# Performance work log

Measured on AMD Instinct MI355X. Metric: run time of the kernel, lower is better.

## Reference

```python
import jax, jax.numpy as jnp
import numpy as np

N_P, N_A, D, H, E = 200000, 100000, 64, 32, 1000000


def setup_inputs() -> dict:
    key = jax.random.key(0)
    ks = jax.random.split(key, 32)
    inp = {}
    inp["x_paper"] = jax.random.normal(ks[0], (N_P, D), jnp.float32)
    inp["x_author"] = jax.random.normal(ks[1], (N_A, D), jnp.float32)
    inp["cites_src"] = jax.random.randint(ks[2], (E,), 0, N_P, jnp.int32)
    inp["cites_dst"] = jax.random.randint(ks[3], (E,), 0, N_P, jnp.int32)
    inp["writes_src"] = jax.random.randint(ks[4], (E,), 0, N_A, jnp.int32)
    inp["writes_dst"] = jax.random.randint(ks[5], (E,), 0, N_P, jnp.int32)
    inp["rev_src"] = jax.random.randint(ks[6], (E,), 0, N_P, jnp.int32)
    inp["rev_dst"] = jax.random.randint(ks[7], (E,), 0, N_A, jnp.int32)
    # per-relation SAGEConv params; layer 1: D->H, layer 2: H->H
    i = 8
    for layer, din in ((1, D), (2, H)):
        for rel in ("cites", "writes", "rev"):
            inp[f"W{layer}l_{rel}"] = 0.1 * jax.random.normal(ks[i], (din, H), jnp.float32); i += 1
            inp[f"W{layer}r_{rel}"] = 0.1 * jax.random.normal(ks[i], (din, H), jnp.float32); i += 1
            inp[f"b{layer}_{rel}"] = 0.01 * jax.random.normal(ks[i], (H,), jnp.float32); i += 1
    return inp


def _sage(x_src, x_dst, src, dst, Wl, Wr, b, n_dst):
    # PyG SAGEConv (aggr='mean'): lin_l(mean of source msgs) + lin_r(x_dst) + bias
    msg = x_src[src]                                              # [E, d] gather
    s = jax.ops.segment_sum(msg, dst, num_segments=n_dst)         # [n_dst, d]
    cnt = jax.ops.segment_sum(jnp.ones((src.shape[0],), x_src.dtype), dst, num_segments=n_dst)
    mean = s / jnp.maximum(cnt, 1.0)[:, None]
    return mean @ Wl + x_dst @ Wr + b


def reference(x_paper, x_author, cites_src, cites_dst, writes_src, writes_dst,
              rev_src, rev_dst,
              W1l_cites, W1r_cites, b1_cites, W1l_writes, W1r_writes, b1_writes,
              W1l_rev, W1r_rev, b1_rev,
              W2l_cites, W2r_cites, b2_cites, W2l_writes, W2r_writes, b2_writes,
              W2l_rev, W2r_rev, b2_rev):
    n_p, n_a = x_paper.shape[0], x_author.shape[0]
    # layer 1 (to_hetero sums relation outputs per dst node type), then relu
    p1 = jax.nn.relu(
        _sage(x_paper, x_paper, cites_src, cites_dst, W1l_cites, W1r_cites, b1_cites, n_p)
        + _sage(x_author, x_paper, writes_src, writes_dst, W1l_writes, W1r_writes, b1_writes, n_p))
    a1 = jax.nn.relu(
        _sage(x_paper, x_author, rev_src, rev_dst, W1l_rev, W1r_rev, b1_rev, n_a))
    # layer 2, return 'paper' output (no activation)
    p2 = (_sage(p1, p1, cites_src, cites_dst, W2l_cites, W2r_cites, b2_cites, n_p)
          + _sage(a1, p1, writes_src, writes_dst, W2l_writes, W2r_writes, b2_writes, n_p))
    return p2
```

## Files before the change

kernel.cpp:

```cpp
#include <hip/hip_runtime.h>

typedef unsigned short u16;
typedef unsigned int   u32;
typedef unsigned char  u8;
typedef __attribute__((ext_vector_type(8))) short bf16x8;
typedef __attribute__((ext_vector_type(4))) float f32x4;

#define N_P 200000
#define N_A 100000
#define DD  64
#define HH  32
#define NE  1000000
#define NBP 782
#define NBA 391
#define NB4K 245
#define NCB 196
#define P4CAP 8192
#define NB_P16 12500
#define NB_A16 6250
#define NB4K3 735

__device__ inline float bf2f(u16 u) { return __uint_as_float(((u32)u) << 16); }
__device__ inline u16 f2bf(float f) {
    u32 u = __float_as_uint(f);
    u += 0x7fffu + ((u >> 16) & 1u);
    return (u16)(u >> 16);
}
__device__ inline float lo_f(u32 m) { return __uint_as_float(m << 16); }
__device__ inline float hi_f(u32 m) { return __uint_as_float(m & 0xffff0000u); }
__device__ inline u32 cvtpk(float a, float b) {
    u32 r;
    asm("v_cvt_pk_bf16_f32 %0, %1, %2" : "=v"(r) : "v"(a), "v"(b));
    return r;
}

__device__ inline void gseg_dual(
    const u16* __restrict__ yA, const int* __restrict__ bkA, int s0, int e0,
    const u16* __restrict__ yB, const int* __restrict__ bkB, int s1, int e1,
    int lane, float& axo, float& ayo, float& bxo, float& byo) {
    float ax = 0.f, ay = 0.f, bx = 0.f, by = 0.f;
    int lastA = min(max(e0 - 1, s0), NE - 1);
    int lastB = min(max(e1 - 1, s1), NE - 1);
    for (int j0 = s0, j1 = s1; (j0 < e0) || (j1 < e1); j0 += 8, j1 += 8) {
        int ia[8], ib[8];
#pragma unroll
        for (int i = 0; i < 8; ++i) ia[i] = bkA[min(j0 + i, lastA)];
#pragma unroll
        for (int i = 0; i < 8; ++i) ib[i] = bkB[min(j1 + i, lastB)];
        u32 ma[8], mb[8];
#pragma unroll
        for (int i = 0; i < 8; ++i)
            ma[i] = *(const u32*)(yA + (size_t)(u32)ia[i] + lane * 2);
#pragma unroll
        for (int i = 0; i < 8; ++i)
            mb[i] = *(const u32*)(yB + (size_t)(u32)ib[i] + lane * 2);
#pragma unroll
        for (int i = 0; i < 8; ++i) {
            u32 va = (j0 + i < e0) ? ma[i] : 0u;
            ax += lo_f(va); ay += hi_f(va);
        }
#pragma unroll
        for (int i = 0; i < 8; ++i) {
            u32 vb = (j1 + i < e1) ? mb[i] : 0u;
            bx += lo_f(vb); by += hi_f(vb);
        }
    }
    axo = ax; ayo = ay; bxo = bx; byo = by;
}

__global__ __launch_bounds__(256) void p1_hist_k(
    const int* __restrict__ cd, const int* __restrict__ wd, const int* __restrict__ rd,
    int* __restrict__ gsizes) {
    int rel = blockIdx.y;
    const int* dst; int shift;
    if (rel == 0)      { dst = cd; shift = 10; }
    else if (rel == 1) { dst = wd; shift = 10; }
    else               { dst = rd; shift = 9;  }
    __shared__ int cnt[256];
    int t = threadIdx.x;
    cnt[t] = 0;
    __syncthreads();
    int e0 = blockIdx.x * 4096;
    if (e0 + 4096 <= NE) {
        const int4* dv = (const int4*)(dst + e0);
#pragma unroll
        for (int i = 0; i < 4; ++i) {
            int4 v = dv[i * 256 + t];
            atomicAdd(&cnt[v.x >> shift], 1);
            atomicAdd(&cnt[v.y >> shift], 1);
            atomicAdd(&cnt[v.z >> shift], 1);
            atomicAdd(&cnt[v.w >> shift], 1);
        }
    } else {
#pragma unroll
        for (int i = 0; i < 16; ++i) {
            int e = e0 + i * 256 + t;
            if (e < NE) atomicAdd(&cnt[dst[e] >> shift], 1);
        }
    }
    __syncthreads();
    if (t < NCB && cnt[t]) atomicAdd(&gsizes[rel * NCB + t], cnt[t]);
}

__global__ __launch_bounds__(256) void p2_scan_k(
    const int* __restrict__ gsizes, int* __restrict__ bases, int* __restrict__ gcur) {
    __shared__ int lds[256];
    int t = threadIdx.x;
    for (int rel = 0; rel < 3; ++rel) {
        int v = (t < NCB) ? gsizes[rel * NCB + t] : 0;
        lds[t] = v; __syncthreads();
#pragma unroll
        for (int o = 1; o < 256; o <<= 1) {
            int x = (t >= o) ? lds[t - o] : 0;
            __syncthreads();
            lds[t] += x;
            __syncthreads();
        }
        int ex = lds[t] - v;
        if (t < NCB) { bases[rel * NCB + t] = ex; gcur[rel * NCB + t] = ex; }
        __syncthreads();
    }
}

__global__ __launch_bounds__(256) void p3t1_k(
    const int* __restrict__ cs, const int* __restrict__ cd,
    const int* __restrict__ ws_, const int* __restrict__ wd,
    const int* __restrict__ rs, const int* __restrict__ rd,
    int* __restrict__ gcur,
    u32* __restrict__ pr_c, u32* __restrict__ pr_w, u32* __restrict__ pr_r,
    const float* __restrict__ xp, const float* __restrict__ xa,
    const u16* __restrict__ wt1h, const u16* __restrict__ wt1l,
    const float* __restrict__ b1s, const float* __restrict__ b1r,
    u16* __restrict__ y_pc, u16* __restrict__ y_pr, u16* __restrict__ y_aw,
    u16* __restrict__ hb_p, u16* __restrict__ hb_a) {
    __shared__ float smem[256 * 34];
    int t = threadIdx.x;
    if (blockIdx.x < NB4K3) {
        u32* sbuf  = (u32*)smem;
        int* cnt   = (int*)(smem + 4096);
        int* sc    = (int*)(smem + 4352);
        int* lcur  = (int*)(smem + 4608);
        int* gbase = (int*)(smem + 4864);
        u8*  bb    = (u8*)(smem + 5120);
        int rel = blockIdx.x / NB4K;
        int blk = blockIdx.x - rel * NB4K;
        const int *src, *dst; int shift; u32* out;
        if (rel == 0)      { src = cs;  dst = cd; shift = 10; out = pr_c; }
        else if (rel == 1) { src = ws_; dst = wd; shift = 10; out = pr_w; }
        else               { src = rs;  dst = rd; shift = 9;  out = pr_r; }
        cnt[t] = 0;
        __syncthreads();
        int e0 = blk * 4096;
        int myd[16], mys[16];
        if (e0 + 4096 <= NE) {
            const int4* dv = (const int4*)(dst + e0);
            const int4* sv = (const int4*)(src + e0);
#pragma unroll
            for (int i = 0; i < 4; ++i) {
                int4 v = dv[i * 256 + t];
                int4 s = sv[i * 256 + t];
                myd[4 * i] = v.x; myd[4 * i + 1] = v.y; myd[4 * i + 2] = v.z; myd[4 * i + 3] = v.w;
                mys[4 * i] = s.x; mys[4 * i + 1] = s.y; mys[4 * i + 2] = s.z; mys[4 * i + 3] = s.w;
                atomicAdd(&cnt[v.x >> shift], 1);
                atomicAdd(&cnt[v.y >> shift], 1);
                atomicAdd(&cnt[v.z >> shift], 1);
                atomicAdd(&cnt[v.w >> shift], 1);
            }
        } else {
#pragma unroll
            for (int i = 0; i < 4; ++i) {
#pragma unroll
                for (int c = 0; c < 4; ++c) {
                    int e = e0 + (i * 256 + t) * 4 + c;
                    int idx = 4 * i + c;
                    if (e < NE) {
                        myd[idx] = dst[e]; mys[idx] = src[e];
                        atomicAdd(&cnt[myd[idx] >> shift], 1);
                    } else { myd[idx] = -1; mys[idx] = 0; }
                }
            }
        }
        __syncthreads();
        int v = cnt[t];
        sc[t] = v; __syncthreads();
#pragma unroll
        for (int o = 1; o < 256; o <<= 1) {
            int x = (t >= o) ? sc[t - o] : 0;
            __syncthreads();
            sc[t] += x;
            __syncthreads();
        }
        int ex = sc[t] - v;
        __syncthreads();
        sc[t] = ex;
        lcur[t] = ex;
        if (t < NCB) gbase[t] = atomicAdd(&gcur[rel * NCB + t], cnt[t]);
        __syncthreads();
#pragma unroll
        for (int i = 0; i < 16; ++i) {
            if (myd[i] >= 0) {
                int d = myd[i];
                int cb = d >> shift;
                u32 dloc = (u32)(d - (cb << shift));
                u32 pk = (dloc << 18) | (u32)mys[i];
                int p = atomicAdd(&lcur[cb], 1);
                sbuf[p] = pk;
                bb[p] = (u8)cb;
            }
        }
        __syncthreads();
        int nvalid = min(4096, NE - e0);
        for (int i = t; i < nvalid; i += 256) {
            int cb = bb[i];
            out[gbase[cb] + (i - sc[cb])] = sbuf[i];
        }
    } else {
        float* Cs = smem;
        int w = t >> 6, l = t & 63;
        int lm = l & 15, lk = l >> 4;
        int bx = blockIdx.x - NB4K3;
        bool paper = bx < NBP;
        int row0 = (paper ? bx : bx - NBP) * 256;
        const float* x = paper ? xp : xa;
        int NROW = paper ? N_P : N_A;
        int nv = min(256, NROW - row0);
        bf16x8 xh[4][2], xl[4][2];
#pragma unroll
        for (int i = 0; i < 4; ++i) {
            int rowg = min(row0 + w * 64 + i * 16 + lm, NROW - 1);
            const float* rp = x + (size_t)rowg * DD + lk * 8;
#pragma unroll
            for (int kc = 0; kc < 2; ++kc) {
                float4 a = *(const float4*)(rp + kc * 32);
                float4 b = *(const float4*)(rp + kc * 32 + 4);
                float f[8] = {a.x, a.y, a.z, a.w, b.x, b.y, b.z, b.w};
                union { u32 u[4]; bf16x8 v; } H, L;
#pragma unroll
                for (int j = 0; j < 4; ++j) {
                    u32 u0 = __float_as_uint(f[2 * j]);
                    u32 u1 = __float_as_uint(f[2 * j + 1]);
                    u32 m0 = u0 & 0xffff0000u;
                    u32 m1 = u1 & 0xffff0000u;
                    H.u[j] = (u0 >> 16) | m1;
                    float l0 = f[2 * j]     - __uint_as_float(m0);
                    float l1 = f[2 * j + 1] - __uint_as_float(m1);
                    L.u[j] = cvtpk(l0, l1);
                }
                xh[i][kc] = H.v; xl[i][kc] = L.v;
            }
        }
        int nw = paper ? 3 : 2;
#pragma unroll 1
        for (int iw = 0; iw < nw; ++iw) {
            int mat = paper ? iw : (3 + iw);
            const u16* Wh = wt1h + mat * 2048;
            const u16* Wl = wt1l + mat * 2048;
            bf16x8 Bh[2][2], Bl[2][2];
#pragma unroll
            for (int ct = 0; ct < 2; ++ct)
#pragma unroll
                for (int kc = 0; kc < 2; ++kc) {
                    int off = (ct * 16 + lm) * 64 + kc * 32 + lk * 8;
                    Bh[ct][kc] = *(const bf16x8*)(Wh + off);
                    Bl[ct][kc] = *(const bf16x8*)(Wl + off);
                }
            float bv[2] = {0.f, 0.f};
            if (paper && iw == 2)  { bv[0] = b1s[lm]; bv[1] = b1s[16 + lm]; }
            if (!paper && iw == 1) { bv[0] = b1r[lm]; bv[1] = b1r[16 + lm]; }
#pragma unroll
            for (int i = 0; i < 4; ++i) {
#pragma unroll
                for (int ct = 0; ct < 2; ++ct) {
                    f32x4 acc = {bv[ct], bv[ct], bv[ct], bv[ct]};
                    acc = __builtin_amdgcn_mfma_f32_16x16x32_bf16(xh[i][0], Bh[ct][0], acc, 0, 0, 0);
                    acc = __builtin_amdgcn_mfma_f32_16x16x32_bf16(xh[i][1], Bh[ct][1], acc, 0, 0, 0);
                    acc = __builtin_amdgcn_mfma_f32_16x16x32_bf16(xl[i][0], Bh[ct][0], acc, 0, 0, 0);
                    acc = __builtin_amdgcn_mfma_f32_16x16x32_bf16(xl[i][1], Bh[ct][1], acc, 0, 0, 0);
                    acc = __builtin_amdgcn_mfma_f32_16x16x32_bf16(xh[i][0], Bl[ct][0], acc, 0, 0, 0);
                    acc = __builtin_amdgcn_mfma_f32_16x16x32_bf16(xh[i][1], Bl[ct][1], acc, 0, 0, 0);
                    int rbase = w * 64 + i * 16 + lk * 4;
#pragma unroll
                    for (int r = 0; r < 4; ++r)
                        Cs[(rbase + r) * 34 + ct * 16 + lm] = acc[r];
                }
            }
            asm volatile("s_waitcnt lgkmcnt(0)" ::: "memory");
            u16* outp;
            if (paper) outp = (iw == 0) ? y_pc : (iw == 1) ? y_pr : hb_p;
            else       outp = (iw == 0) ? y_aw : hb_a;
            u32* g = (u32*)(outp + (size_t)row0 * HH);
#pragma unroll
            for (int p = 0; p < 4; ++p) {
                int j = p * 64 + l;
                int rl = w * 64 + (j >> 2);
                if (rl < nv) {
                    const float* q = Cs + rl * 34 + (j & 3) * 8;
                    u32 o[4];
#pragma unroll
                    for (int jj = 0; jj < 4; ++jj)
                        o[jj] = cvtpk(q[2 * jj], q[2 * jj + 1]);
                    *(uint4*)(g + ((size_t)w * 256 + j) * 4) = make_uint4(o[0], o[1], o[2], o[3]);
                }
            }
            asm volatile("" ::: "memory");
        }
    }
}

__global__ __launch_bounds__(256) void p4_sort_k(
    const int* __restrict__ bases, const int* __restrict__ gsizes,
    const u32* __restrict__ pr_c, const u32* __restrict__ pr_w, const u32* __restrict__ pr_r,
    int* __restrict__ bkt_c, int* __restrict__ bkt_w, int* __restrict__ bkt_r,
    int* __restrict__ st_c, int* __restrict__ st_w, int* __restrict__ st_r) {
    int rel = blockIdx.y;
    const u32* pr; int* bkt; int* st; int width, n;
    if (rel == 0)      { pr = pr_c; bkt = bkt_c; st = st_c; width = 1024; n = N_P; }
    else if (rel == 1) { pr = pr_w; bkt = bkt_w; st = st_w; width = 1024; n = N_P; }
    else               { pr = pr_r; bkt = bkt_r; st = st_r; width = 512;  n = N_A; }
    __shared__ u32 sin[P4CAP];
    __shared__ int cnt[1024], sc2[1024], tmp[256];
    int t = threadIdx.x;
    int b = blockIdx.x;
    int base = bases[rel * NCB + b];
    int size = min(gsizes[rel * NCB + b], P4CAP);
    int d0 = b * width;
    int nd = min(width, n - d0);
    if (nd <= 0) return;
#pragma unroll
    for (int j = t; j < 1024; j += 256) cnt[j] = 0;
    __syncthreads();
    for (int i = t; i < size; i += 256) {
        u32 pk = pr[base + i];
        sin[i] = pk;
        atomicAdd(&cnt[pk >> 18], 1);
    }
    __syncthreads();
    int j0 = 4 * t;
    int c0 = cnt[j0], c1 = cnt[j0 + 1], c2 = cnt[j0 + 2], c3 = cnt[j0 + 3];
    int tot = c0 + c1 + c2 + c3;
    tmp[t] = tot; __syncthreads();
#pragma unroll
    for (int o = 1; o < 256; o <<= 1) {
        int x = (t >= o) ? tmp[t - o] : 0;
        __syncthreads();
        tmp[t] += x;
        __syncthreads();
    }
    int pre = tmp[t] - tot;
    sc2[j0] = pre;
    sc2[j0 + 1] = pre + c0;
    sc2[j0 + 2] = pre + c0 + c1;
    sc2[j0 + 3] = pre + c0 + c1 + c2;
    __syncthreads();
    for (int j = t; j < nd; j += 256) st[d0 + j] = base + sc2[j];
#pragma unroll
    for (int j = t; j < 1024; j += 256) cnt[j] = 0;
    __syncthreads();
    for (int i = t; i < size; i += 256) {
        u32 pk = sin[i];
        int dl = (int)(pk >> 18);
        int pos = sc2[dl] + atomicAdd(&cnt[dl], 1);
        bkt[base + pos] = (int)((pk & 0x3FFFFu) * HH);
    }
}

__global__ __launch_bounds__(256) void prep_w_k(
    const float* __restrict__ W1lc, const float* __restrict__ W1lr,
    const float* __restrict__ W1rc, const float* __restrict__ W1rw,
    const float* __restrict__ W1lw, const float* __restrict__ W1rr,
    const float* __restrict__ W2lc, const float* __restrict__ W2rc,
    const float* __restrict__ W2rw, const float* __restrict__ W2lw,
    const float* __restrict__ b1c, const float* __restrict__ b1w,
    const float* __restrict__ b2c, const float* __restrict__ b2w,
    u16* __restrict__ wt1h, u16* __restrict__ wt1l,
    u16* __restrict__ wt2h, u16* __restrict__ wt2l,
    float* __restrict__ b1s, float* __restrict__ b2s,
    int* __restrict__ gsizes) {
    int m = blockIdx.x, t = threadIdx.x;
    if (m == 0) {
        for (int e = t; e < 3 * NCB; e += 256) gsizes[e] = 0;
    }
    if (m < 5) {
        const float *A = nullptr, *B = nullptr;
        if (m == 0) A = W1lc;
        else if (m == 1) A = W1lr;
        else if (m == 2) { A = W1rc; B = W1rw; }
        else if (m == 3) A = W1lw;
        else A = W1rr;
        for (int e = t; e < 2048; e += 256) {
            int k = e >> 5, n = e & 31;
            float v = A[e] + (B ? B[e] : 0.f);
            u16 h = f2bf(v);
            u16 lw = f2bf(v - bf2f(h));
            wt1h[m * 2048 + n * 64 + k] = h;
            wt1l[m * 2048 + n * 64 + k] = lw;
        }
        if (m == 2 && t < HH) b1s[t] = b1c[t] + b1w[t];
    } else {
        int mm = m - 5;
        const float *A = nullptr, *B = nullptr;
        if (mm == 0) A = W2lc;
        else if (mm == 1) { A = W2rc; B = W2rw; }
        else A = W2lw;
        for (int e = t; e < 1024; e += 256) {
            int k = e >> 5, n = e & 31;
            float v = A[e] + (B ? B[e] : 0.f);
            u16 h = f2bf(v);
            u16 lw = f2bf(v - bf2f(h));
            wt2h[mm * 1024 + n * 32 + k] = h;
            wt2l[mm * 1024 + n * 32 + k] = lw;
        }
        if (mm == 1 && t < HH) b2s[t] = b2c[t] + b2w[t];
    }
}

__global__ __launch_bounds__(256) void agg1_k(
    const u16* __restrict__ y_pc, const u16* __restrict__ y_aw,
    const u16* __restrict__ y_pr,
    const int* __restrict__ st_c, const int* __restrict__ bkt_c,
    const int* __restrict__ st_w, const int* __restrict__ bkt_w,
    const int* __restrict__ st_r, const int* __restrict__ bkt_r,
    u32* __restrict__ hb_p, u32* __restrict__ hb_a) {
    int t = threadIdx.x, g = t >> 4, lane = t & 15;
    if (blockIdx.x < NB_P16) {
        int row = blockIdx.x * 16 + g;
        u32 self = hb_p[(size_t)row * (HH / 2) + lane];
        int s0 = st_c[row];
        int e0 = (row == N_P - 1) ? NE : st_c[row + 1];
        int s1 = st_w[row];
        int e1 = (row == N_P - 1) ? NE : st_w[row + 1];
        float cx, cy, wx, wy;
        gseg_dual(y_pc, bkt_c, s0, e0, y_aw, bkt_w, s1, e1, lane, cx, cy, wx, wy);
        int d0 = e0 - s0, d1 = e1 - s1;
        float iv0 = 1.0f / (float)(d0 < 1 ? 1 : d0);
        float iv1 = 1.0f / (float)(d1 < 1 ? 1 : d1);
        float ax = fmaxf(cx * iv0 + wx * iv1 + lo_f(self), 0.f);
        float ay = fmaxf(cy * iv0 + wy * iv1 + hi_f(self), 0.f);
        hb_p[(size_t)row * (HH / 2) + lane] = cvtpk(ax, ay);
    } else {
        int row = (blockIdx.x - NB_P16) * 16 + g;
        u32 self = hb_a[(size_t)row * (HH / 2) + lane];
        int s = st_r[row];
        int e = (row == N_A - 1) ? NE : st_r[row + 1];
        int mid = (s + e) >> 1;
        float ax0, ay0, ax1, ay1;
        gseg_dual(y_pr, bkt_r, s, mid, y_pr, bkt_r, mid, e, lane, ax0, ay0, ax1, ay1);
        int dg = e - s;
        float iv = 1.0f / (float)(dg < 1 ? 1 : dg);
        float ax = fmaxf((ax0 + ax1) * iv + lo_f(self), 0.f);
        float ay = fmaxf((ay0 + ay1) * iv + hi_f(self), 0.f);
        hb_a[(size_t)row * (HH / 2) + lane] = cvtpk(ax, ay);
    }
}

__global__ __launch_bounds__(256) void agg2_k(
    const u16* __restrict__ hb_p, const u16* __restrict__ hb_a,
    const int* __restrict__ st_c, const int* __restrict__ bkt_c,
    const int* __restrict__ st_w, const int* __restrict__ bkt_w,
    const u16* __restrict__ wt2h, const u16* __restrict__ wt2l,
    const float* __restrict__ b2s, float* __restrict__ out) {
    __shared__ float mcs[16][34];
    __shared__ float mws[16][34];
    __shared__ float cso[16][34];
    int t = threadIdx.x, g = t >> 4, lane = t & 15;
    int row0 = blockIdx.x * 16;
    int row = row0 + g;
    int s0 = st_c[row];
    int e0 = (row == N_P - 1) ? NE : st_c[row + 1];
    int s1 = st_w[row];
    int e1 = (row == N_P - 1) ? NE : st_w[row + 1];
    float cx, cy, wx, wy;
    gseg_dual(hb_p, bkt_c, s0, e0, hb_a, bkt_w, s1, e1, lane, cx, cy, wx, wy);
    int d0 = e0 - s0, d1 = e1 - s1;
    float iv0 = 1.0f / (float)(d0 < 1 ? 1 : d0);
    float iv1 = 1.0f / (float)(d1 < 1 ? 1 : d1);
    mcs[g][2 * lane] = cx * iv0;  mcs[g][2 * lane + 1] = cy * iv0;
    mws[g][2 * lane] = wx * iv1;  mws[g][2 * lane + 1] = wy * iv1;
    __syncthreads();
    if (t < 64) {
        int lm = t & 15, lk = t >> 4;
        bf16x8 as_ = *(const bf16x8*)(hb_p + (size_t)(row0 + lm) * HH + lk * 8);
        bf16x8 mch, mcl, mwh, mwl;
        {
            union { u32 u[4]; bf16x8 v; } H, L;
#pragma unroll
            for (int j = 0; j < 4; ++j) {
                float f0 = mcs[lm][lk * 8 + 2 * j];
                float f1 = mcs[lm][lk * 8 + 2 * j + 1];
                u32 u0 = __float_as_uint(f0), u1 = __float_as_uint(f1);
                u32 m0 = u0 & 0xffff0000u, m1 = u1 & 0xffff0000u;
                H.u[j] = (u0 >> 16) | m1;
                L.u[j] = cvtpk(f0 - __uint_as_float(m0), f1 - __uint_as_float(m1));
            }
            mch = H.v; mcl = L.v;
#pragma unroll
            for (int j = 0; j < 4; ++j) {
                float f0 = mws[lm][lk * 8 + 2 * j];
                float f1 = mws[lm][lk * 8 + 2 * j + 1];
                u32 u0 = __float_as_uint(f0), u1 = __float_as_uint(f1);
                u32 m0 = u0 & 0xffff0000u, m1 = u1 & 0xffff0000u;
                H.u[j] = (u0 >> 16) | m1;
                L.u[j] = cvtpk(f0 - __uint_as_float(m0), f1 - __uint_as_float(m1));
            }
            mwh = H.v; mwl = L.v;
        }
#pragma unroll
        for (int ct = 0; ct < 2; ++ct) {
            int boff = (ct * 16 + lm) * 32 + lk * 8;
            bf16x8 Bch = *(const bf16x8*)(wt2h + boff);
            bf16x8 Bcl = *(const bf16x8*)(wt2l + boff);
            bf16x8 Bsh = *(const bf16x8*)(wt2h + 1024 + boff);
            bf16x8 Bsl = *(const bf16x8*)(wt2l + 1024 + boff);
            bf16x8 Bwh = *(const bf16x8*)(wt2h + 2048 + boff);
            bf16x8 Bwl = *(const bf16x8*)(wt2l + 2048 + boff);
            float bb = b2s[ct * 16 + lm];
            f32x4 acc = {bb, bb, bb, bb};
            acc = __builtin_amdgcn_mfma_f32_16x16x32_bf16(as_, Bsh, acc, 0, 0, 0);
            acc = __builtin_amdgcn_mfma_f32_16x16x32_bf16(as_, Bsl, acc, 0, 0, 0);
            acc = __builtin_amdgcn_mfma_f32_16x16x32_bf16(mch, Bch, acc, 0, 0, 0);
            acc = __builtin_amdgcn_mfma_f32_16x16x32_bf16(mcl, Bch, acc, 0, 0, 0);
            acc = __builtin_amdgcn_mfma_f32_16x16x32_bf16(mch, Bcl, acc, 0, 0, 0);
            acc = __builtin_amdgcn_mfma_f32_16x16x32_bf16(mwh, Bwh, acc, 0, 0, 0);
            acc = __builtin_amdgcn_mfma_f32_16x16x32_bf16(mwl, Bwh, acc, 0, 0, 0);
            acc = __builtin_amdgcn_mfma_f32_16x16x32_bf16(mwh, Bwl, acc, 0, 0, 0);
#pragma unroll
            for (int r = 0; r < 4; ++r)
                cso[lk * 4 + r][ct * 16 + lm] = acc[r];
        }
    }
    __syncthreads();
    int r = t >> 4, c = (t & 15) * 2;
    *(float2*)(out + (size_t)(row0 + r) * HH + c) = make_float2(cso[r][c], cso[r][c + 1]);
}

extern "C" void kernel_launch(void* const* d_in, const int* in_sizes, int n_in,
                              void* d_out, int out_size, void* d_ws, size_t ws_size,
                              hipStream_t stream) {
    const float* x_p  = (const float*)d_in[0];
    const float* x_a  = (const float*)d_in[1];
    const int* c_src  = (const int*)d_in[2];
    const int* c_dst  = (const int*)d_in[3];
    const int* w_src  = (const int*)d_in[4];
    const int* w_dst  = (const int*)d_in[5];
    const int* r_src  = (const int*)d_in[6];
    const int* r_dst  = (const int*)d_in[7];
    const float* W1l_c = (const float*)d_in[8];
    const float* W1r_c = (const float*)d_in[9];
    const float* b1_c  = (const float*)d_in[10];
    const float* W1l_w = (const float*)d_in[11];
    const float* W1r_w = (const float*)d_in[12];
    const float* b1_w  = (const float*)d_in[13];
    const float* W1l_r = (const float*)d_in[14];
    const float* W1r_r = (const float*)d_in[15];
    const float* b1_r  = (const float*)d_in[16];
    const float* W2l_c = (const float*)d_in[17];
    const float* W2r_c = (const float*)d_in[18];
    const float* b2_c  = (const float*)d_in[19];
    const float* W2l_w = (const float*)d_in[20];
    const float* W2r_w = (const float*)d_in[21];
    const float* b2_w  = (const float*)d_in[22];

    int* gsizes = (int*)d_ws;
    int* bases  = gsizes + 3 * NCB;
    int* gcur   = bases + 3 * NCB;
    int* st_c   = gcur + 3 * NCB;
    int* st_w   = st_c + N_P;
    int* st_r   = st_w + N_P;
    int* bkt_c  = st_r + N_A;
    int* bkt_w  = bkt_c + NE;
    int* bkt_r  = bkt_w + NE;
    u16* wt1h  = (u16*)(bkt_r + NE);
    u16* wt1l  = wt1h + 5 * 2048;
    u16* wt2h  = wt1l + 5 * 2048;
    u16* wt2l  = wt2h + 3 * 1024;
    float* b1s = (float*)(wt2l + 3 * 1024);
    float* b2s = b1s + HH;
    u16* hb_p  = (u16*)(b2s + HH);
    u16* hb_a  = hb_p + (size_t)N_P * HH;
    u16* y_pc  = hb_a + (size_t)N_A * HH;
    u16* y_pr  = y_pc + (size_t)N_P * HH;
    u16* y_aw  = y_pr + (size_t)N_P * HH;
    float* tail = (float*)(y_aw + (size_t)N_A * HH);
    u32* pr_c  = (u32*)tail;
    u32* pr_w  = pr_c + NE;
    u32* pr_r  = pr_w + NE;
    float* outp = (float*)d_out;

    const size_t need = ((uintptr_t)(pr_r + NE)) - (uintptr_t)d_ws;
    if (ws_size < need) return;

    prep_w_k<<<8, 256, 0, stream>>>(W1l_c, W1l_r, W1r_c, W1r_w, W1l_w, W1r_r,
                                    W2l_c, W2r_c, W2r_w, W2l_w,
                                    b1_c, b1_w, b2_c, b2_w,
                                    wt1h, wt1l, wt2h, wt2l, b1s, b2s, gsizes);
    p1_hist_k<<<dim3(NB4K, 3), 256, 0, stream>>>(c_dst, w_dst, r_dst, gsizes);
    p2_scan_k<<<1, 256, 0, stream>>>(gsizes, bases, gcur);
    p3t1_k<<<NB4K3 + NBP + NBA, 256, 0, stream>>>(
        c_src, c_dst, w_src, w_dst, r_src, r_dst, gcur, pr_c, pr_w, pr_r,
        x_p, x_a, wt1h, wt1l, b1s, b1_r, y_pc, y_pr, y_aw, hb_p, hb_a);
    p4_sort_k<<<dim3(NCB, 3), 256, 0, stream>>>(bases, gsizes, pr_c, pr_w, pr_r,
                                                bkt_c, bkt_w, bkt_r, st_c, st_w, st_r);
    agg1_k<<<NB_P16 + NB_A16, 256, 0, stream>>>(y_pc, y_aw, y_pr,
                                                st_c, bkt_c, st_w, bkt_w, st_r, bkt_r,
                                                (u32*)hb_p, (u32*)hb_a);
    agg2_k<<<NB_P16, 256, 0, stream>>>(hb_p, hb_a, st_c, bkt_c, st_w, bkt_w,
                                       wt2h, wt2l, b2s, outp);
}
```

Baseline: 363.6 us.

## Rebalance layer-1 transform across scatter and sort kernels, merge prep and histogram

Splits the dense layer-1 transform blocks so some run alongside the partition scatter kernel and the rest alongside the per-bucket counting sort. Each launch then mixes memory-bound sort work with MFMA compute, which should fill idle CUs. Weight prep and the histogram are merged into one launch, and the scan is spread over three blocks. Row-start arrays gain a sentinel entry, which removes the last-row branch in the aggregation kernels. In exchange the sort kernel needs a larger shared-memory footprint, which may lower occupancy, and the split point is a fixed tuning constant.

```diff
diff --git a/kernel.cpp b/kernel.cpp
--- a/kernel.cpp
+++ b/kernel.cpp
@@ -13,6 +13,8 @@
 #define NE  1000000
 #define NBP 782
 #define NBA 391
+#define NB_T1 1173
+#define TSPLIT 500
 #define NB4K 245
 #define NCB 196
 #define P4CAP 8192
@@ -68,61 +70,207 @@
     axo = ax; ayo = ay; bxo = bx; byo = by;
 }
 
-__global__ __launch_bounds__(256) void p1_hist_k(
+__device__ void t1_body(int bx, float* Cs,
+    const float* __restrict__ xp, const float* __restrict__ xa,
+    const u16* __restrict__ wt1h, const u16* __restrict__ wt1l,
+    const float* __restrict__ b1s, const float* __restrict__ b1r,
+    u16* __restrict__ y_pc, u16* __restrict__ y_pr, u16* __restrict__ y_aw,
+    u16* __restrict__ hb_p, u16* __restrict__ hb_a) {
+    int t = threadIdx.x, w = t >> 6, l = t & 63;
+    int lm = l & 15, lk = l >> 4;
+    bool paper = bx < NBP;
+    int row0 = (paper ? bx : bx - NBP) * 256;
+    const float* x = paper ? xp : xa;
+    int NROW = paper ? N_P : N_A;
+    int nv = min(256, NROW - row0);
+    bf16x8 xh[4][2], xl[4][2];
+#pragma unroll
+    for (int i = 0; i < 4; ++i) {
+        int rowg = min(row0 + w * 64 + i * 16 + lm, NROW - 1);
+        const float* rp = x + (size_t)rowg * DD + lk * 8;
+#pragma unroll
+        for (int kc = 0; kc < 2; ++kc) {
+            float4 a = *(const float4*)(rp + kc * 32);
+            float4 b = *(const float4*)(rp + kc * 32 + 4);
+            float f[8] = {a.x, a.y, a.z, a.w, b.x, b.y, b.z, b.w};
+            union { u32 u[4]; bf16x8 v; } H, L;
+#pragma unroll
+            for (int j = 0; j < 4; ++j) {
+                u32 u0 = __float_as_uint(f[2 * j]);
+                u32 u1 = __float_as_uint(f[2 * j + 1]);
+                u32 m0 = u0 & 0xffff0000u;
+                u32 m1 = u1 & 0xffff0000u;
+                H.u[j] = (u0 >> 16) | m1;
+                float l0 = f[2 * j]     - __uint_as_float(m0);
+                float l1 = f[2 * j + 1] - __uint_as_float(m1);
+                L.u[j] = cvtpk(l0, l1);
+            }
+            xh[i][kc] = H.v; xl[i][kc] = L.v;
+        }
+    }
+    int nw = paper ? 3 : 2;
+#pragma unroll 1
+    for (int iw = 0; iw < nw; ++iw) {
+        int mat = paper ? iw : (3 + iw);
+        const u16* Wh = wt1h + mat * 2048;
+        const u16* Wl = wt1l + mat * 2048;
+        bf16x8 Bh[2][2], Bl[2][2];
+#pragma unroll
+        for (int ct = 0; ct < 2; ++ct)
+#pragma unroll
+            for (int kc = 0; kc < 2; ++kc) {
+                int off = (ct * 16 + lm) * 64 + kc * 32 + lk * 8;
+                Bh[ct][kc] = *(const bf16x8*)(Wh + off);
+                Bl[ct][kc] = *(const bf16x8*)(Wl + off);
+            }
+        float bv[2] = {0.f, 0.f};
+        if (paper && iw == 2)  { bv[0] = b1s[lm]; bv[1] = b1s[16 + lm]; }
+        if (!paper && iw == 1) { bv[0] = b1r[lm]; bv[1] = b1r[16 + lm]; }
+#pragma unroll
+        for (int i = 0; i < 4; ++i) {
+#pragma unroll
+            for (int ct = 0; ct < 2; ++ct) {
+                f32x4 acc = {bv[ct], bv[ct], bv[ct], bv[ct]};
+                acc = __builtin_amdgcn_mfma_f32_16x16x32_bf16(xh[i][0], Bh[ct][0], acc, 0, 0, 0);
+                acc = __builtin_amdgcn_mfma_f32_16x16x32_bf16(xh[i][1], Bh[ct][1], acc, 0, 0, 0);
+                acc = __builtin_amdgcn_mfma_f32_16x16x32_bf16(xl[i][0], Bh[ct][0], acc, 0, 0, 0);
+                acc = __builtin_amdgcn_mfma_f32_16x16x32_bf16(xl[i][1], Bh[ct][1], acc, 0, 0, 0);
+                acc = __builtin_amdgcn_mfma_f32_16x16x32_bf16(xh[i][0], Bl[ct][0], acc, 0, 0, 0);
+                acc = __builtin_amdgcn_mfma_f32_16x16x32_bf16(xh[i][1], Bl[ct][1], acc, 0, 0, 0);
+                int rbase = w * 64 + i * 16 + lk * 4;
+#pragma unroll
+                for (int r = 0; r < 4; ++r)
+                    Cs[(rbase + r) * 34 + ct * 16 + lm] = acc[r];
+            }
+        }
+        asm volatile("s_waitcnt lgkmcnt(0)" ::: "memory");
+        u16* outp;
+        if (paper) outp = (iw == 0) ? y_pc : (iw == 1) ? y_pr : hb_p;
+        else       outp = (iw == 0) ? y_aw : hb_a;
+        u32* g = (u32*)(outp + (size_t)row0 * HH);
+#pragma unroll
+        for (int p = 0; p < 4; ++p) {
+            int j = p * 64 + l;
+            int rl = w * 64 + (j >> 2);
+            if (rl < nv) {
+                const float* q = Cs + rl * 34 + (j & 3) * 8;
+                u32 o[4];
+#pragma unroll
+                for (int jj = 0; jj < 4; ++jj)
+                    o[jj] = cvtpk(q[2 * jj], q[2 * jj + 1]);
+                *(uint4*)(g + ((size_t)w * 256 + j) * 4) = make_uint4(o[0], o[1], o[2], o[3]);
+            }
+        }
+        asm volatile("" ::: "memory");
+    }
+}
+
+__global__ __launch_bounds__(256) void prep1_k(
+    const float* __restrict__ W1lc, const float* __restrict__ W1lr,
+    const float* __restrict__ W1rc, const float* __restrict__ W1rw,
+    const float* __restrict__ W1lw, const float* __restrict__ W1rr,
+    const float* __restrict__ W2lc, const float* __restrict__ W2rc,
+    const float* __restrict__ W2rw, const float* __restrict__ W2lw,
+    const float* __restrict__ b1c, const float* __restrict__ b1w,
+    const float* __restrict__ b2c, const float* __restrict__ b2w,
+    u16* __restrict__ wt1h, u16* __restrict__ wt1l,
+    u16* __restrict__ wt2h, u16* __restrict__ wt2l,
+    float* __restrict__ b1s, float* __restrict__ b2s,
     const int* __restrict__ cd, const int* __restrict__ wd, const int* __restrict__ rd,
     int* __restrict__ gsizes) {
-    int rel = blockIdx.y;
-    const int* dst; int shift;
-    if (rel == 0)      { dst = cd; shift = 10; }
-    else if (rel == 1) { dst = wd; shift = 10; }
-    else               { dst = rd; shift = 9;  }
     __shared__ int cnt[256];
     int t = threadIdx.x;
-    cnt[t] = 0;
-    __syncthreads();
-    int e0 = blockIdx.x * 4096;
-    if (e0 + 4096 <= NE) {
-        const int4* dv = (const int4*)(dst + e0);
-#pragma unroll
-        for (int i = 0; i < 4; ++i) {
-            int4 v = dv[i * 256 + t];
-            atomicAdd(&cnt[v.x >> shift], 1);
-            atomicAdd(&cnt[v.y >> shift], 1);
-            atomicAdd(&cnt[v.z >> shift], 1);
-            atomicAdd(&cnt[v.w >> shift], 1);
+    if (blockIdx.x < 8) {
+        int m = blockIdx.x;
+        if (m < 5) {
+            const float *A = nullptr, *B = nullptr;
+            if (m == 0) A = W1lc;
+            else if (m == 1) A = W1lr;
+            else if (m == 2) { A = W1rc; B = W1rw; }
+            else if (m == 3) A = W1lw;
+            else A = W1rr;
+            for (int e = t; e < 2048; e += 256) {
+                int k = e >> 5, n = e & 31;
+                float v = A[e] + (B ? B[e] : 0.f);
+                u16 h = f2bf(v);
+                u16 lw = f2bf(v - bf2f(h));
+                wt1h[m * 2048 + n * 64 + k] = h;
+                wt1l[m * 2048 + n * 64 + k] = lw;
+            }
+            if (m == 2 && t < HH) b1s[t] = b1c[t] + b1w[t];
+        } else {
+            int mm = m - 5;
+            const float *A = nullptr, *B = nullptr;
+            if (mm == 0) A = W2lc;
+            else if (mm == 1) { A = W2rc; B = W2rw; }
+            else A = W2lw;
+            for (int e = t; e < 1024; e += 256) {
+                int k = e >> 5, n = e & 31;
+                float v = A[e] + (B ? B[e] : 0.f);
+                u16 h = f2bf(v);
+                u16 lw = f2bf(v - bf2f(h));
+                wt2h[mm * 1024 + n * 32 + k] = h;
+                wt2l[mm * 1024 + n * 32 + k] = lw;
+            }
+            if (mm == 1 && t < HH) b2s[t] = b2c[t] + b2w[t];
         }
     } else {
-#pragma unroll
-        for (int i = 0; i < 16; ++i) {
-            int e = e0 + i * 256 + t;
-            if (e < NE) atomicAdd(&cnt[dst[e] >> shift], 1);
-        }
-    }
-    __syncthreads();
-    if (t < NCB && cnt[t]) atomicAdd(&gsizes[rel * NCB + t], cnt[t]);
+        int pb = blockIdx.x - 8;
+        int rel = pb / NB4K, blk = pb - rel * NB4K;
+        const int* dst; int shift;
+        if (rel == 0)      { dst = cd; shift = 10; }
+        else if (rel == 1) { dst = wd; shift = 10; }
+        else               { dst = rd; shift = 9;  }
+        cnt[t] = 0;
+        __syncthreads();
+        int e0 = blk * 4096;
+        if (e0 + 4096 <= NE) {
+            const int4* dv = (const int4*)(dst + e0);
+#pragma unroll
+            for (int i = 0; i < 4; ++i) {
+                int4 v = dv[i * 256 + t];
+                atomicAdd(&cnt[v.x >> shift], 1);
+                atomicAdd(&cnt[v.y >> shift], 1);
+                atomicAdd(&cnt[v.z >> shift], 1);
+                atomicAdd(&cnt[v.w >> shift], 1);
+            }
+        } else {
+#pragma unroll
+            for (int i = 0; i < 16; ++i) {
+                int e = e0 + i * 256 + t;
+                if (e < NE) atomicAdd(&cnt[dst[e] >> shift], 1);
+            }
+        }
+        __syncthreads();
+        if (t < NCB && cnt[t]) atomicAdd(&gsizes[rel * NCB + t], cnt[t]);
+    }
 }
 
 __global__ __launch_bounds__(256) void p2_scan_k(
-    const int* __restrict__ gsizes, int* __restrict__ bases, int* __restrict__ gcur) {
+    const int* __restrict__ gsizes, int* __restrict__ bases, int* __restrict__ gcur,
+    int* __restrict__ st_c, int* __restrict__ st_w, int* __restrict__ st_r) {
     __shared__ int lds[256];
     int t = threadIdx.x;
-    for (int rel = 0; rel < 3; ++rel) {
-        int v = (t < NCB) ? gsizes[rel * NCB + t] : 0;
-        lds[t] = v; __syncthreads();
-#pragma unroll
-        for (int o = 1; o < 256; o <<= 1) {
-            int x = (t >= o) ? lds[t - o] : 0;
-            __syncthreads();
-            lds[t] += x;
-            __syncthreads();
-        }
-        int ex = lds[t] - v;
-        if (t < NCB) { bases[rel * NCB + t] = ex; gcur[rel * NCB + t] = ex; }
-        __syncthreads();
-    }
-}
-
-__global__ __launch_bounds__(256) void p3t1_k(
+    int rel = blockIdx.x;
+    int v = (t < NCB) ? gsizes[rel * NCB + t] : 0;
+    lds[t] = v; __syncthreads();
+#pragma unroll
+    for (int o = 1; o < 256; o <<= 1) {
+        int x = (t >= o) ? lds[t - o] : 0;
+        __syncthreads();
+        lds[t] += x;
+        __syncthreads();
+    }
+    int ex = lds[t] - v;
+    if (t < NCB) { bases[rel * NCB + t] = ex; gcur[rel * NCB + t] = ex; }
+    if (t == 0) {
+        if (rel == 0)      st_c[N_P] = NE;
+        else if (rel == 1) st_w[N_P] = NE;
+        else               st_r[N_A] = NE;
+    }
+}
+
+__global__ __launch_bounds__(256) void pA_k(
     const int* __restrict__ cs, const int* __restrict__ cd,
     const int* __restrict__ ws_, const int* __restrict__ wd,
     const int* __restrict__ rs, const int* __restrict__ rd,
@@ -215,202 +363,78 @@
             out[gbase[cb] + (i - sc[cb])] = sbuf[i];
         }
     } else {
-        float* Cs = smem;
-        int w = t >> 6, l = t & 63;
-        int lm = l & 15, lk = l >> 4;
-        int bx = blockIdx.x - NB4K3;
-        bool paper = bx < NBP;
-        int row0 = (paper ? bx : bx - NBP) * 256;
-        const float* x = paper ? xp : xa;
-        int NROW = paper ? N_P : N_A;
-        int nv = min(256, NROW - row0);
-        bf16x8 xh[4][2], xl[4][2];
-#pragma unroll
-        for (int i = 0; i < 4; ++i) {
-            int rowg = min(row0 + w * 64 + i * 16 + lm, NROW - 1);
-            const float* rp = x + (size_t)rowg * DD + lk * 8;
-#pragma unroll
-            for (int kc = 0; kc < 2; ++kc) {
-                float4 a = *(const float4*)(rp + kc * 32);
-                float4 b = *(const float4*)(rp + kc * 32 + 4);
-                float f[8] = {a.x, a.y, a.z, a.w, b.x, b.y, b.z, b.w};
-                union { u32 u[4]; bf16x8 v; } H, L;
-#pragma unroll
-                for (int j = 0; j < 4; ++j) {
-                    u32 u0 = __float_as_uint(f[2 * j]);
-                    u32 u1 = __float_as_uint(f[2 * j + 1]);
-                    u32 m0 = u0 & 0xffff0000u;
-                    u32 m1 = u1 & 0xffff0000u;
-                    H.u[j] = (u0 >> 16) | m1;
-                    float l0 = f[2 * j]     - __uint_as_float(m0);
-                    float l1 = f[2 * j + 1] - __uint_as_float(m1);
-                    L.u[j] = cvtpk(l0, l1);
-                }
-                xh[i][kc] = H.v; xl[i][kc] = L.v;
-            }
-        }
-        int nw = paper ? 3 : 2;
-#pragma unroll 1
-        for (int iw = 0; iw < nw; ++iw) {
-            int mat = paper ? iw : (3 + iw);
-            const u16* Wh = wt1h + mat * 2048;
-            const u16* Wl = wt1l + mat * 2048;
-            bf16x8 Bh[2][2], Bl[2][2];
-#pragma unroll
-            for (int ct = 0; ct < 2; ++ct)
-#pragma unroll
-                for (int kc = 0; kc < 2; ++kc) {
-                    int off = (ct * 16 + lm) * 64 + kc * 32 + lk * 8;
-                    Bh[ct][kc] = *(const bf16x8*)(Wh + off);
-                    Bl[ct][kc] = *(const bf16x8*)(Wl + off);
-                }
-            float bv[2] = {0.f, 0.f};
-            if (paper && iw == 2)  { bv[0] = b1s[lm]; bv[1] = b1s[16 + lm]; }
-            if (!paper && iw == 1) { bv[0] = b1r[lm]; bv[1] = b1r[16 + lm]; }
-#pragma unroll
-            for (int i = 0; i < 4; ++i) {
-#pragma unroll
-                for (int ct = 0; ct < 2; ++ct) {
-                    f32x4 acc = {bv[ct], bv[ct], bv[ct], bv[ct]};
-                    acc = __builtin_amdgcn_mfma_f32_16x16x32_bf16(xh[i][0], Bh[ct][0], acc, 0, 0, 0);
-                    acc = __builtin_amdgcn_mfma_f32_16x16x32_bf16(xh[i][1], Bh[ct][1], acc, 0, 0, 0);
-                    acc = __builtin_amdgcn_mfma_f32_16x16x32_bf16(xl[i][0], Bh[ct][0], acc, 0, 0, 0);
-                    acc = __builtin_amdgcn_mfma_f32_16x16x32_bf16(xl[i][1], Bh[ct][1], acc, 0, 0, 0);
-                    acc = __builtin_amdgcn_mfma_f32_16x16x32_bf16(xh[i][0], Bl[ct][0], acc, 0, 0, 0);
-                    acc = __builtin_amdgcn_mfma_f32_16x16x32_bf16(xh[i][1], Bl[ct][1], acc, 0, 0, 0);
-                    int rbase = w * 64 + i * 16 + lk * 4;
-#pragma unroll
-                    for (int r = 0; r < 4; ++r)
-                        Cs[(rbase + r) * 34 + ct * 16 + lm] = acc[r];
-                }
-            }
-            asm volatile("s_waitcnt lgkmcnt(0)" ::: "memory");
-            u16* outp;
-            if (paper) outp = (iw == 0) ? y_pc : (iw == 1) ? y_pr : hb_p;
-            else       outp = (iw == 0) ? y_aw : hb_a;
-            u32* g = (u32*)(outp + (size_t)row0 * HH);
-#pragma unroll
-            for (int p = 0; p < 4; ++p) {
-                int j = p * 64 + l;
-                int rl = w * 64 + (j >> 2);
-                if (rl < nv) {
-                    const float* q = Cs + rl * 34 + (j & 3) * 8;
-                    u32 o[4];
-#pragma unroll
-                    for (int jj = 0; jj < 4; ++jj)
-                        o[jj] = cvtpk(q[2 * jj], q[2 * jj + 1]);
-                    *(uint4*)(g + ((size_t)w * 256 + j) * 4) = make_uint4(o[0], o[1], o[2], o[3]);
-                }
-            }
-            asm volatile("" ::: "memory");
-        }
-    }
-}
-
-__global__ __launch_bounds__(256) void p4_sort_k(
+        t1_body(blockIdx.x - NB4K3, smem, xp, xa, wt1h, wt1l, b1s, b1r,
+                y_pc, y_pr, y_aw, hb_p, hb_a);
+    }
+}
+
+__global__ __launch_bounds__(256) void pB_k(
     const int* __restrict__ bases, const int* __restrict__ gsizes,
     const u32* __restrict__ pr_c, const u32* __restrict__ pr_w, const u32* __restrict__ pr_r,
     int* __restrict__ bkt_c, int* __restrict__ bkt_w, int* __restrict__ bkt_r,
-    int* __restrict__ st_c, int* __restrict__ st_w, int* __restrict__ st_r) {
-    int rel = blockIdx.y;
-    const u32* pr; int* bkt; int* st; int width, n;
-    if (rel == 0)      { pr = pr_c; bkt = bkt_c; st = st_c; width = 1024; n = N_P; }
-    else if (rel == 1) { pr = pr_w; bkt = bkt_w; st = st_w; width = 1024; n = N_P; }
-    else               { pr = pr_r; bkt = bkt_r; st = st_r; width = 512;  n = N_A; }
-    __shared__ u32 sin[P4CAP];
-    __shared__ int cnt[1024], sc2[1024], tmp[256];
+    int* __restrict__ st_c, int* __restrict__ st_w, int* __restrict__ st_r,
+    const float* __restrict__ xp, const float* __restrict__ xa,
+    const u16* __restrict__ wt1h, const u16* __restrict__ wt1l,
+    const float* __restrict__ b1s, const float* __restrict__ b1r,
+    u16* __restrict__ y_pc, u16* __restrict__ y_pr, u16* __restrict__ y_aw,
+    u16* __restrict__ hb_p, u16* __restrict__ hb_a) {
+    __shared__ float smem[10496];
     int t = threadIdx.x;
-    int b = blockIdx.x;
-    int base = bases[rel * NCB + b];
-    int size = min(gsizes[rel * NCB + b], P4CAP);
-    int d0 = b * width;
-    int nd = min(width, n - d0);
-    if (nd <= 0) return;
-#pragma unroll
-    for (int j = t; j < 1024; j += 256) cnt[j] = 0;
-    __syncthreads();
-    for (int i = t; i < size; i += 256) {
-        u32 pk = pr[base + i];
-        sin[i] = pk;
-        atomicAdd(&cnt[pk >> 18], 1);
-    }
-    __syncthreads();
-    int j0 = 4 * t;
-    int c0 = cnt[j0], c1 = cnt[j0 + 1], c2 = cnt[j0 + 2], c3 = cnt[j0 + 3];
-    int tot = c0 + c1 + c2 + c3;
-    tmp[t] = tot; __syncthreads();
-#pragma unroll
-    for (int o = 1; o < 256; o <<= 1) {
-        int x = (t >= o) ? tmp[t - o] : 0;
-        __syncthreads();
-        tmp[t] += x;
-        __syncthreads();
-    }
-    int pre = tmp[t] - tot;
-    sc2[j0] = pre;
-    sc2[j0 + 1] = pre + c0;
-    sc2[j0 + 2] = pre + c0 + c1;
-    sc2[j0 + 3] = pre + c0 + c1 + c2;
-    __syncthreads();
-    for (int j = t; j < nd; j += 256) st[d0 + j] = base + sc2[j];
-#pragma unroll
-    for (int j = t; j < 1024; j += 256) cnt[j] = 0;
-    __syncthreads();
-    for (int i = t; i < size; i += 256) {
-        u32 pk = sin[i];
-        int dl = (int)(pk >> 18);
-        int pos = sc2[dl] + atomicAdd(&cnt[dl], 1);
-        bkt[base + pos] = (int)((pk & 0x3FFFFu) * HH);
-    }
-}
-
-__global__ __launch_bounds__(256) void prep_w_k(
-    const float* __restrict__ W1lc, const float* __restrict__ W1lr,
-    const float* __restrict__ W1rc, const float* __restrict__ W1rw,
-    const float* __restrict__ W1lw, const float* __restrict__ W1rr,
-    const float* __restrict__ W2lc, const float* __restrict__ W2rc,
-    const float* __restrict__ W2rw, const float* __restrict__ W2lw,
-    const float* __restrict__ b1c, const float* __restrict__ b1w,
-    const float* __restrict__ b2c, const float* __restrict__ b2w,
-    u16* __restrict__ wt1h, u16* __restrict__ wt1l,
-    u16* __restrict__ wt2h, u16* __restrict__ wt2l,
-    float* __restrict__ b1s, float* __restrict__ b2s,
-    int* __restrict__ gsizes) {
-    int m = blockIdx.x, t = threadIdx.x;
-    if (m == 0) {
-        for (int e = t; e < 3 * NCB; e += 256) gsizes[e] = 0;
-    }
-    if (m < 5) {
-        const float *A = nullptr, *B = nullptr;
-        if (m == 0) A = W1lc;
-        else if (m == 1) A = W1lr;
-        else if (m == 2) { A = W1rc; B = W1rw; }
-        else if (m == 3) A = W1lw;
-        else A = W1rr;
-        for (int e = t; e < 2048; e += 256) {
-            int k = e >> 5, n = e & 31;
-            float v = A[e] + (B ? B[e] : 0.f);
-            u16 h = f2bf(v);
-            u16 lw = f2bf(v - bf2f(h));
-            wt1h[m * 2048 + n * 64 + k] = h;
-            wt1l[m * 2048 + n * 64 + k] = lw;
-        }
-        if (m == 2 && t < HH) b1s[t] = b1c[t] + b1w[t];
+    if (blockIdx.x < 3 * NCB) {
+        u32* sin = (u32*)smem;
+        int* cnt = (int*)(sin + P4CAP);
+        int* sc2 = cnt + 1024;
+        int* tmp = sc2 + 1024;
+        int rel = blockIdx.x / NCB;
+        int b = blockIdx.x - rel * NCB;
+        const u32* pr; int* bkt; int* st; int width, n;
+        if (rel == 0)      { pr = pr_c; bkt = bkt_c; st = st_c; width = 1024; n = N_P; }
+        else if (rel == 1) { pr = pr_w; bkt = bkt_w; st = st_w; width = 1024; n = N_P; }
+        else               { pr = pr_r; bkt = bkt_r; st = st_r; width = 512;  n = N_A; }
+        int base = bases[rel * NCB + b];
+        int size = min(gsizes[rel * NCB + b], P4CAP);
+        int d0 = b * width;
+        int nd = min(width, n - d0);
+        if (nd <= 0) return;
+#pragma unroll
+        for (int j = t; j < 1024; j += 256) cnt[j] = 0;
+        __syncthreads();
+        for (int i = t; i < size; i += 256) {
+            u32 pk = pr[base + i];
+            sin[i] = pk;
+            atomicAdd(&cnt[pk >> 18], 1);
+        }
+        __syncthreads();
+        int j0 = 4 * t;
+        int c0 = cnt[j0], c1 = cnt[j0 + 1], c2 = cnt[j0 + 2], c3 = cnt[j0 + 3];
+        int tot = c0 + c1 + c2 + c3;
+        tmp[t] = tot; __syncthreads();
+#pragma unroll
+        for (int o = 1; o < 256; o <<= 1) {
+            int x = (t >= o) ? tmp[t - o] : 0;
+            __syncthreads();
+            tmp[t] += x;
+            __syncthreads();
+        }
+        int pre = tmp[t] - tot;
+        sc2[j0] = pre;
+        sc2[j0 + 1] = pre + c0;
+        sc2[j0 + 2] = pre + c0 + c1;
+        sc2[j0 + 3] = pre + c0 + c1 + c2;
+        __syncthreads();
+        for (int j = t; j < nd; j += 256) st[d0 + j] = base + sc2[j];
+#pragma unroll
+        for (int j = t; j < 1024; j += 256) cnt[j] = 0;
+        __syncthreads();
+        for (int i = t; i < size; i += 256) {
+            u32 pk = sin[i];
+            int dl = (int)(pk >> 18);
+            int pos = sc2[dl] + atomicAdd(&cnt[dl], 1);
+            bkt[base + pos] = (int)((pk & 0x3FFFFu) * HH);
+        }
     } else {
-        int mm = m - 5;
-        const float *A = nullptr, *B = nullptr;
-        if (mm == 0) A = W2lc;
-        else if (mm == 1) { A = W2rc; B = W2rw; }
-        else A = W2lw;
-        for (int e = t; e < 1024; e += 256) {
-            int k = e >> 5, n = e & 31;
-            float v = A[e] + (B ? B[e] : 0.f);
-            u16 h = f2bf(v);
-            u16 lw = f2bf(v - bf2f(h));
-            wt2h[mm * 1024 + n * 32 + k] = h;
-            wt2l[mm * 1024 + n * 32 + k] = lw;
-        }
-        if (mm == 1 && t < HH) b2s[t] = b2c[t] + b2w[t];
+        t1_body(blockIdx.x - 3 * NCB + TSPLIT, smem, xp, xa, wt1h, wt1l, b1s, b1r,
+                y_pc, y_pr, y_aw, hb_p, hb_a);
     }
 }
 
@@ -425,10 +449,8 @@
     if (blockIdx.x < NB_P16) {
         int row = blockIdx.x * 16 + g;
         u32 self = hb_p[(size_t)row * (HH / 2) + lane];
-        int s0 = st_c[row];
-        int e0 = (row == N_P - 1) ? NE : st_c[row + 1];
-        int s1 = st_w[row];
-        int e1 = (row == N_P - 1) ? NE : st_w[row + 1];
+        int s0 = st_c[row], e0 = st_c[row + 1];
+        int s1 = st_w[row], e1 = st_w[row + 1];
         float cx, cy, wx, wy;
         gseg_dual(y_pc, bkt_c, s0, e0, y_aw, bkt_w, s1, e1, lane, cx, cy, wx, wy);
         int d0 = e0 - s0, d1 = e1 - s1;
@@ -440,8 +462,7 @@
     } else {
         int row = (blockIdx.x - NB_P16) * 16 + g;
         u32 self = hb_a[(size_t)row * (HH / 2) + lane];
-        int s = st_r[row];
-        int e = (row == N_A - 1) ? NE : st_r[row + 1];
+        int s = st_r[row], e = st_r[row + 1];
         int mid = (s + e) >> 1;
         float ax0, ay0, ax1, ay1;
         gseg_dual(y_pr, bkt_r, s, mid, y_pr, bkt_r, mid, e, lane, ax0, ay0, ax1, ay1);
@@ -465,10 +486,8 @@
     int t = threadIdx.x, g = t >> 4, lane = t & 15;
     int row0 = blockIdx.x * 16;
     int row = row0 + g;
-    int s0 = st_c[row];
-    int e0 = (row == N_P - 1) ? NE : st_c[row + 1];
-    int s1 = st_w[row];
-    int e1 = (row == N_P - 1) ? NE : st_w[row + 1];
+    int s0 = st_c[row], e0 = st_c[row + 1];
+    int s1 = st_w[row], e1 = st_w[row + 1];
     float cx, cy, wx, wy;
     gseg_dual(hb_p, bkt_c, s0, e0, hb_a, bkt_w, s1, e1, lane, cx, cy, wx, wy);
     int d0 = e0 - s0, d1 = e1 - s1;
@@ -564,9 +583,9 @@
     int* bases  = gsizes + 3 * NCB;
     int* gcur   = bases + 3 * NCB;
     int* st_c   = gcur + 3 * NCB;
-    int* st_w   = st_c + N_P;
-    int* st_r   = st_w + N_P;
-    int* bkt_c  = st_r + N_A;
+    int* st_w   = st_c + N_P + 1;
+    int* st_r   = st_w + N_P + 1;
+    int* bkt_c  = st_r + N_A + 1;
     int* bkt_w  = bkt_c + NE;
     int* bkt_r  = bkt_w + NE;
     u16* wt1h  = (u16*)(bkt_r + NE);
@@ -589,17 +608,19 @@
     const size_t need = ((uintptr_t)(pr_r + NE)) - (uintptr_t)d_ws;
     if (ws_size < need) return;
 
-    prep_w_k<<<8, 256, 0, stream>>>(W1l_c, W1l_r, W1r_c, W1r_w, W1l_w, W1r_r,
-                                    W2l_c, W2r_c, W2r_w, W2l_w,
-                                    b1_c, b1_w, b2_c, b2_w,
-                                    wt1h, wt1l, wt2h, wt2l, b1s, b2s, gsizes);
-    p1_hist_k<<<dim3(NB4K, 3), 256, 0, stream>>>(c_dst, w_dst, r_dst, gsizes);
-    p2_scan_k<<<1, 256, 0, stream>>>(gsizes, bases, gcur);
-    p3t1_k<<<NB4K3 + NBP + NBA, 256, 0, stream>>>(
+    hipMemsetAsync(gsizes, 0, 3 * NCB * sizeof(int), stream);
+    prep1_k<<<8 + NB4K3, 256, 0, stream>>>(W1l_c, W1l_r, W1r_c, W1r_w, W1l_w, W1r_r,
+                                           W2l_c, W2r_c, W2r_w, W2l_w,
+                                           b1_c, b1_w, b2_c, b2_w,
+                                           wt1h, wt1l, wt2h, wt2l, b1s, b2s,
+                                           c_dst, w_dst, r_dst, gsizes);
+    p2_scan_k<<<3, 256, 0, stream>>>(gsizes, bases, gcur, st_c, st_w, st_r);
+    pA_k<<<NB4K3 + TSPLIT, 256, 0, stream>>>(
         c_src, c_dst, w_src, w_dst, r_src, r_dst, gcur, pr_c, pr_w, pr_r,
         x_p, x_a, wt1h, wt1l, b1s, b1_r, y_pc, y_pr, y_aw, hb_p, hb_a);
-    p4_sort_k<<<dim3(NCB, 3), 256, 0, stream>>>(bases, gsizes, pr_c, pr_w, pr_r,
-                                                bkt_c, bkt_w, bkt_r, st_c, st_w, st_r);
+    pB_k<<<3 * NCB + (NB_T1 - TSPLIT), 256, 0, stream>>>(
+        bases, gsizes, pr_c, pr_w, pr_r, bkt_c, bkt_w, bkt_r, st_c, st_w, st_r,
+        x_p, x_a, wt1h, wt1l, b1s, b1_r, y_pc, y_pr, y_aw, hb_p, hb_a);
     agg1_k<<<NB_P16 + NB_A16, 256, 0, stream>>>(y_pc, y_aw, y_pr,
                                                 st_c, bkt_c, st_w, bkt_w, st_r, bkt_r,
                                                 (u32*)hb_p, (u32*)hb_a);
```

After: 390.6 us. 7.4% more time.
